# Optimization experiments

Hardware: AMD Instinct MI355X
Metric: run time of the kernel (lower is better)

## Reference

```python
import jax, jax.numpy as jnp
import numpy as np

S, B, D, H, K, M, MEM = 1024, 2, 1024, 16, 64, 4096, 1
T = (MEM + 1) * S  # key length = (mem_len+1)*seq_len


def setup_inputs() -> dict:
    key = jax.random.key(0)
    ks = jax.random.split(key, 16)

    def w(k, shape):  # N(0, 0.02) init as in the torch module
        return jax.random.normal(k, shape, dtype=jnp.float32) * 0.02

    x = jax.random.normal(ks[0], (S, B, D), dtype=jnp.float32)
    p = jax.random.normal(ks[1], (T, B, D), dtype=jnp.float32)
    memory = jax.random.normal(ks[2], (MEM * S, B, D), dtype=jnp.float32)
    u_bias = w(ks[3], (H, K))
    v_bias = w(ks[4], (H, K))
    # Transformer-XL causal mask: query s may attend to keys t <= mem_len*S + s
    t_idx = jnp.arange(T)[None, :]
    s_idx = jnp.arange(S)[:, None]
    mask = jnp.where(t_idx <= MEM * S + s_idx, 0.0, -1e9).astype(jnp.float32)[None]  # [1,S,T]
    return {
        "x": x, "p": p, "mask": mask, "memory": memory,
        "u_bias": u_bias, "v_bias": v_bias,
        "wq_w": w(ks[5], (H * K, D)), "wke_w": w(ks[6], (H * K, D)),
        "wkr_w": w(ks[7], (H * K, D)), "wv_w": w(ks[8], (H * K, D)),
        "wc_w": w(ks[9], (D, H * K)),
        "w1_w": w(ks[10], (M, D)), "w1_b": jnp.zeros((M,), jnp.float32),
        "w2_w": w(ks[11], (D, M)), "w2_b": jnp.zeros((D,), jnp.float32),
        "ln1_g": jnp.ones((D,), jnp.float32), "ln1_b": jnp.zeros((D,), jnp.float32),
        "ln2_g": jnp.ones((D,), jnp.float32), "ln2_b": jnp.zeros((D,), jnp.float32),
    }


def _layernorm(x, g, b, eps=1e-5):
    mu = jnp.mean(x, axis=-1, keepdims=True)
    var = jnp.mean(jnp.square(x - mu), axis=-1, keepdims=True)
    return (x - mu) / jnp.sqrt(var + eps) * g + b


def reference(x, p, mask, memory, u_bias, v_bias,
              wq_w, wke_w, wkr_w, wv_w, wc_w,
              w1_w, w1_b, w2_w, w2_b, ln1_g, ln1_b, ln2_g, ln2_b):
    s_len, b_sz, d = x.shape
    q = (x @ wq_w.T).reshape(s_len, b_sz, H, K)            # [S,B,H,K]
    x_mem = jnp.concatenate([memory, x], axis=0)           # [T,B,D]
    k_e = (x_mem @ wke_w.T).reshape(T, b_sz, H, K)         # content keys
    k_r = (p @ wkr_w.T).reshape(T, b_sz, H, K)             # relative-position keys
    v = (x_mem @ wv_w.T).reshape(T, b_sz, H, K)
    # AC: content score, BD: relative-position score (Transformer-XL)
    ac = jnp.einsum("sbhk,tbhk->bhst", q + u_bias, k_e)
    bd = jnp.einsum("sbhk,tbhk->bhst", q + v_bias, k_r)
    alpha = (ac + bd) / np.sqrt(K).astype(np.float32) + mask[:, None]  # [B,H,S,T]
    alpha = jax.nn.softmax(alpha, axis=-1)
    av = jnp.einsum("bhst,tbhk->sbhk", alpha, v).reshape(s_len, b_sz, H * K)
    u = av @ wc_w.T
    u = _layernorm(u + x, ln1_g, ln1_b)
    z = jax.nn.relu(u @ w1_w.T + w1_b) @ w2_w.T + w2_b
    z = _layernorm(z + u, ln2_g, ln2_b)
    return z
```

## Files before the change

kernel.cpp:

```cpp
#include <hip/hip_runtime.h>
#include <math.h>

#define S_LEN 1024
#define BATCH 2
#define DM 1024
#define NH 16
#define HD 64
#define FFN_DIM 4096
#define RQ 2048
#define RT 4096
#define T_LEN 2048
#define KROW 72
#define NPART 4
#define OPSTR 2097152L

typedef __attribute__((ext_vector_type(8))) short short8;
typedef __attribute__((ext_vector_type(4))) float f32x4;

__device__ __forceinline__ unsigned short f2bf(float f) {
    unsigned u = __builtin_bit_cast(unsigned, f);
    u += 0x7fffu + ((u >> 16) & 1u);
    return (unsigned short)(u >> 16);
}
__device__ __forceinline__ float bf2f(unsigned short s) { return __builtin_bit_cast(float, ((unsigned)s) << 16); }

#define GLD_LDS16(gptr, lptr)                                                                  \
    __builtin_amdgcn_global_load_lds((const __attribute__((address_space(1))) unsigned int*)(gptr), \
                                     (__attribute__((address_space(3))) unsigned int*)(lptr), 16, 0, 0)

__device__ __forceinline__ ushort4 cvt4(float4 v) {
    ushort4 o;
    o.x = f2bf(v.x); o.y = f2bf(v.y); o.z = f2bf(v.z); o.w = f2bf(v.w);
    return o;
}

__global__ void cast_all_kernel(const float* __restrict__ wq, const float* __restrict__ wke,
                                const float* __restrict__ wv, const float* __restrict__ wkr,
                                const float* __restrict__ wc, const float* __restrict__ w1,
                                const float* __restrict__ w2, const float* __restrict__ x,
                                const float* __restrict__ p, const float* __restrict__ mem,
                                unsigned short* __restrict__ wdst, unsigned short* __restrict__ xbf,
                                unsigned short* __restrict__ pbf, unsigned short* __restrict__ xm) {
    const long Q = 256 * 1024;
    const long W = 13 * Q;
    long i = (long)blockIdx.x * blockDim.x + threadIdx.x;
    if (i < W) {
        const float* src; long off;
        if      (i < 1 * Q) { src = wq;  off = 0; }
        else if (i < 2 * Q) { src = wke; off = 1 * Q; }
        else if (i < 3 * Q) { src = wv;  off = 2 * Q; }
        else if (i < 4 * Q) { src = wkr; off = 3 * Q; }
        else if (i < 5 * Q) { src = wc;  off = 4 * Q; }
        else if (i < 9 * Q) { src = w1;  off = 5 * Q; }
        else                { src = w2;  off = 9 * Q; }
        ((ushort4*)wdst)[i] = cvt4(((const float4*)src)[i - off]);
    } else if (i < W + 2 * Q) {
        long j = i - W;
        ((ushort4*)xbf)[j] = cvt4(((const float4*)x)[j]);
    } else if (i < W + 6 * Q) {
        long j = i - W - 2 * Q;
        ((ushort4*)pbf)[j] = cvt4(((const float4*)p)[j]);
    } else {
        long j = i - W - 6 * Q;
        float4 v = (j < 2 * Q) ? ((const float4*)mem)[j] : ((const float4*)x)[j - 2 * Q];
        ((ushort4*)xm)[j] = cvt4(v);
    }
}

#define BM 128
#define BN 128
#define GBK 64
#define PBK 32

__launch_bounds__(256)
__global__ void proj_fused(const unsigned short* __restrict__ xbf, const unsigned short* __restrict__ xmbf,
                           const unsigned short* __restrict__ pbf, const unsigned short* __restrict__ wqb,
                           const unsigned short* __restrict__ wkevb, const unsigned short* __restrict__ wkrb,
                           unsigned short* __restrict__ qo, unsigned short* __restrict__ keo,
                           unsigned short* __restrict__ vTo, unsigned short* __restrict__ kro) {
    __shared__ __align__(16) short As[BM * PBK];
    __shared__ __align__(16) short Bs[BN * PBK];
    const int id = blockIdx.x;
    const unsigned short *A, *B;
    unsigned short *Yb, *Yv = nullptr;
    int bx, by;
    if (id < 128)      { A = xbf;  B = wqb;   Yb = qo;  bx = id & 7;   by = id >> 3; }
    else if (id < 640) { int t = id - 128; A = xmbf; B = wkevb; Yb = keo; Yv = vTo;
                         bx = t & 15; by = t >> 4; }
    else               { int t = id - 640; A = pbf;  B = wkrb;  Yb = kro;
                         bx = t & 7;  by = t >> 3; }
    const int tid = threadIdx.x;
    const int w = tid >> 6, lane = tid & 63;
    const int row0 = by * BM, col0 = bx * BN;
    const int wr = (w >> 1) * 64, wcn = (w & 1) * 64;
    f32x4 acc[4][4] = {};
    const int lrow = lane & 15, quad = lane >> 4;
    for (int k0 = 0; k0 < DM; k0 += PBK) {
        __syncthreads();
#pragma unroll
        for (int i = 0; i < 2; ++i) {
            int c = w * 128 + i * 64 + lane;
            int row = c >> 2, kg = c & 3;
            int kl = (kg - (row >> 1)) & 3;
            GLD_LDS16(A + (long)(row0 + row) * DM + k0 + kl * 8, As + (w * 128 + i * 64) * 8);
            GLD_LDS16(B + (long)(col0 + row) * DM + k0 + kl * 8, Bs + (w * 128 + i * 64) * 8);
        }
        __syncthreads();
        short8 a[4], b[4];
#pragma unroll
        for (int mi = 0; mi < 4; ++mi) {
            int r = wr + mi * 16 + lrow;
            int ph = (quad + (r >> 1)) & 3;
            a[mi] = *(const short8*)&As[r * PBK + ph * 8];
        }
#pragma unroll
        for (int ni = 0; ni < 4; ++ni) {
            int r = wcn + ni * 16 + lrow;
            int ph = (quad + (r >> 1)) & 3;
            b[ni] = *(const short8*)&Bs[r * PBK + ph * 8];
        }
#pragma unroll
        for (int mi = 0; mi < 4; ++mi)
#pragma unroll
            for (int ni = 0; ni < 4; ++ni)
                acc[mi][ni] = __builtin_amdgcn_mfma_f32_16x16x32_bf16(a[mi], b[ni], acc[mi][ni], 0, 0, 0);
    }
    const int mb = row0 + wr + quad * 4;
    const int nb = col0 + wcn + lrow;
    const bool isv = (Yv != nullptr) && (col0 >= 1024);
#pragma unroll
    for (int mi = 0; mi < 4; ++mi)
#pragma unroll
        for (int ni = 0; ni < 4; ++ni) {
            const int r = mb + mi * 16, cc = nb + ni * 16;
#pragma unroll
            for (int reg = 0; reg < 4; ++reg) {
                float val = acc[mi][ni][reg];
                const int rf = r + reg;
                if (isv) {
                    int c2 = cc - 1024;
                    int t = rf >> 1, b2 = rf & 1;
                    int h2 = c2 >> 6, d2 = c2 & 63;
                    Yv[((long)(b2 * NH + h2) * HD + d2) * T_LEN + t] = f2bf(val);
                } else {
                    Yb[(long)rf * DM + cc] = f2bf(val);
                }
            }
        }
}

__launch_bounds__(256)
__global__ void gemm_mfma(const unsigned short* __restrict__ A, const unsigned short* __restrict__ B,
                          const float* __restrict__ bias,
                          float* __restrict__ of0, float* __restrict__ of1,
                          float* __restrict__ of2, float* __restrict__ of3,
                          unsigned short* __restrict__ Yb, int Kd, int N, int relu,
                          int klen) {
    __shared__ __align__(16) short As[BM * GBK];
    __shared__ __align__(16) short Bs[BN * GBK];
    const int nbx = N >> 7;
    const int cpx = gridDim.x >> 3;
    const int bid = ((blockIdx.x & 7) * cpx) + (blockIdx.x >> 3);
    const int per_z = nbx << 4;
    const int z = bid / per_z;
    const int r2 = bid - z * per_z;
    const int by = r2 / nbx, bx = r2 - by * nbx;
    const int tid = threadIdx.x;
    const int w = tid >> 6, lane = tid & 63;
    const int row0 = by * BM, col0 = bx * BN;
    const int kbeg = z * klen;
    const int wr = (w >> 1) * 64, wcn = (w & 1) * 64;
    f32x4 acc[4][4] = {};
    const int lrow = lane & 15, quad = lane >> 4;
    for (int k0 = kbeg; k0 < kbeg + klen; k0 += GBK) {
        __syncthreads();
#pragma unroll
        for (int i = 0; i < 4; ++i) {
            int c = i * 256 + tid;
            int row = c >> 3, ph = c & 7;
            int kl = (ph - row) & 7;
            GLD_LDS16(A + (long)(row0 + row) * Kd + k0 + kl * 8, As + (i * 256 + w * 64) * 8);
            GLD_LDS16(B + (long)(col0 + row) * Kd + k0 + kl * 8, Bs + (i * 256 + w * 64) * 8);
        }
        __syncthreads();
#pragma unroll
        for (int hh = 0; hh < 2; ++hh) {
            short8 a[4], b[4];
#pragma unroll
            for (int mi = 0; mi < 4; ++mi) {
                int r = wr + mi * 16 + lrow;
                int ph = (hh * 4 + quad + r) & 7;
                a[mi] = *(const short8*)&As[r * GBK + ph * 8];
            }
#pragma unroll
            for (int ni = 0; ni < 4; ++ni) {
                int r = wcn + ni * 16 + lrow;
                int ph = (hh * 4 + quad + r) & 7;
                b[ni] = *(const short8*)&Bs[r * GBK + ph * 8];
            }
#pragma unroll
            for (int mi = 0; mi < 4; ++mi)
#pragma unroll
                for (int ni = 0; ni < 4; ++ni)
                    acc[mi][ni] = __builtin_amdgcn_mfma_f32_16x16x32_bf16(a[mi], b[ni], acc[mi][ni], 0, 0, 0);
        }
    }
    const int mb = row0 + wr + quad * 4;
    const int nb = col0 + wcn + lrow;
    float* of = (z == 0) ? of0 : (z == 1) ? of1 : (z == 2) ? of2 : of3;
    float bb[4];
#pragma unroll
    for (int ni = 0; ni < 4; ++ni) bb[ni] = bias ? bias[nb + ni * 16] : 0.f;
#pragma unroll
    for (int mi = 0; mi < 4; ++mi)
#pragma unroll
        for (int ni = 0; ni < 4; ++ni) {
            const int r = mb + mi * 16, cc = nb + ni * 16;
#pragma unroll
            for (int reg = 0; reg < 4; ++reg) {
                float val = acc[mi][ni][reg] + bb[ni];
                if (relu) val = fmaxf(val, 0.f);
                if (Yb) Yb[(long)(r + reg) * N + cc] = f2bf(val);
                else    of[(long)(r + reg) * N + cc] = val;
            }
        }
}

__launch_bounds__(256)
__global__ void prep_kernel(const unsigned short* __restrict__ kr,
                            const float* __restrict__ ub, const float* __restrict__ vb,
                            unsigned short* __restrict__ ke_io, float* __restrict__ biasg) {
    const int r = blockIdx.x;
    const int tid = threadIdx.x;
    const int h = tid >> 4, seg = tid & 15;
    ushort4 keu = ((const ushort4*)(ke_io + (long)r * DM))[tid];
    ushort4 kru = ((const ushort4*)(kr + (long)r * DM))[tid];
    float ke0 = bf2f(keu.x), ke1 = bf2f(keu.y), ke2 = bf2f(keu.z), ke3 = bf2f(keu.w);
    float kr0 = bf2f(kru.x), kr1 = bf2f(kru.y), kr2 = bf2f(kru.z), kr3 = bf2f(kru.w);
    float4 u4 = ((const float4*)ub)[tid];
    float4 v4 = ((const float4*)vb)[tid];
    ushort4 s;
    s.x = f2bf((ke0 + kr0) * 0.125f); s.y = f2bf((ke1 + kr1) * 0.125f);
    s.z = f2bf((ke2 + kr2) * 0.125f); s.w = f2bf((ke3 + kr3) * 0.125f);
    ((ushort4*)(ke_io + (long)r * DM))[tid] = s;
    float part = u4.x * ke0 + u4.y * ke1 + u4.z * ke2 + u4.w * ke3
               + v4.x * kr0 + v4.y * kr1 + v4.z * kr2 + v4.w * kr3;
    part += __shfl_xor(part, 1);
    part += __shfl_xor(part, 2);
    part += __shfl_xor(part, 4);
    part += __shfl_xor(part, 8);
    if (seg == 0) {
        const int t = r >> 1, b = r & 1;
        biasg[(b * NH + h) * T_LEN + t] = part * 0.125f;
    }
}

__launch_bounds__(256)
__global__ void attn_mfma(const unsigned short* __restrict__ qg,
                          const unsigned short* __restrict__ ksum,
                          const unsigned short* __restrict__ vT,
                          const float* __restrict__ biasg,
                          float* __restrict__ Op01, float* __restrict__ Op2,
                          float* __restrict__ Op3, float2* __restrict__ mlout) {
    __shared__ __align__(16) unsigned short Ks[64 * KROW];
    __shared__ __align__(16) unsigned short Vs[64 * KROW];
    __shared__ __align__(16) unsigned short Ps[4][16 * KROW];
    const int bid0 = blockIdx.x;
    const int bid = (bid0 & 7) * 256 + (bid0 >> 3);
    const int part = bid >> 9, rid = bid & 511;
    const int stile = (rid & 15) ^ 15, h = (rid >> 4) & 15, b = rid >> 8;
    const int tid = threadIdx.x, w = tid >> 6, lane = tid & 63;
    const int L = lane & 15, quad = lane >> 4;
    const int qbase = stile * 64 + w * 16;
    short8 qf0, qf1;
    {
        const unsigned short* qp = qg + ((long)(qbase + L) * 2 + b) * DM + h * HD + quad * 8;
        qf0 = *(const short8*)(qp);
        qf1 = *(const short8*)(qp + 32);
    }
    f32x4 O[4] = {};
    float mrow[4] = {-1e30f, -1e30f, -1e30f, -1e30f};
    float lrow[4] = {0.f, 0.f, 0.f, 0.f};
    const int nch = 17 + stile;
    const float* bias_p = biasg + (long)(b * NH + h) * T_LEN;
    const unsigned short* ks_base = ksum + (long)b * DM + h * HD;
    const unsigned short* vt_base = vT + (long)(b * NH + h) * HD * T_LEN;
    const int c0 = tid, c1 = 256 + tid;
    const int row_a = c0 >> 3, seg_a = c0 & 7;
    const int row_b = c1 >> 3, seg_b = c1 & 7;
    uint4 pk0, pk1, pv0, pv1;
    float pb[4];
    {
        const int tf = part * 64;
        pk0 = *(const uint4*)(ks_base + (long)(tf + row_a) * 2 * DM + seg_a * 8);
        pk1 = *(const uint4*)(ks_base + (long)(tf + row_b) * 2 * DM + seg_b * 8);
        pv0 = *(const uint4*)(vt_base + (long)row_a * T_LEN + tf + seg_a * 8);
        pv1 = *(const uint4*)(vt_base + (long)row_b * T_LEN + tf + seg_b * 8);
#pragma unroll
        for (int kt = 0; kt < 4; ++kt) pb[kt] = bias_p[tf + kt * 16 + L];
    }
    for (int ch = part; ch < nch; ch += NPART) {
        const int t0 = ch * 64;
        __syncthreads();
        *(uint4*)&Ks[row_a * KROW + seg_a * 8] = pk0;
        *(uint4*)&Ks[row_b * KROW + seg_b * 8] = pk1;
        *(uint4*)&Vs[row_a * KROW + seg_a * 8] = pv0;
        *(uint4*)&Vs[row_b * KROW + seg_b * 8] = pv1;
        __syncthreads();
        const bool more = (ch + NPART < nch);
        float pbn[4];
        if (more) {
            const int t1 = t0 + NPART * 64;
            pk0 = *(const uint4*)(ks_base + (long)(t1 + row_a) * 2 * DM + seg_a * 8);
            pk1 = *(const uint4*)(ks_base + (long)(t1 + row_b) * 2 * DM + seg_b * 8);
            pv0 = *(const uint4*)(vt_base + (long)row_a * T_LEN + t1 + seg_a * 8);
            pv1 = *(const uint4*)(vt_base + (long)row_b * T_LEN + t1 + seg_b * 8);
#pragma unroll
            for (int kt = 0; kt < 4; ++kt) pbn[kt] = bias_p[t1 + kt * 16 + L];
        }
        f32x4 S[4] = {};
        __builtin_amdgcn_s_setprio(1);
#pragma unroll
        for (int kt = 0; kt < 4; ++kt) {
            short8 kb0 = *(const short8*)&Ks[(kt * 16 + L) * KROW + quad * 8];
            short8 kb1 = *(const short8*)&Ks[(kt * 16 + L) * KROW + 32 + quad * 8];
            S[kt] = __builtin_amdgcn_mfma_f32_16x16x32_bf16(qf0, kb0, S[kt], 0, 0, 0);
            S[kt] = __builtin_amdgcn_mfma_f32_16x16x32_bf16(qf1, kb1, S[kt], 0, 0, 0);
        }
        __builtin_amdgcn_s_setprio(0);
        float sc[4][4];
        float cm[4] = {-1e30f, -1e30f, -1e30f, -1e30f};
        if (ch != nch - 1) {
#pragma unroll
            for (int kt = 0; kt < 4; ++kt)
#pragma unroll
                for (int reg = 0; reg < 4; ++reg) {
                    float v = S[kt][reg] + pb[kt];
                    sc[kt][reg] = v;
                    cm[reg] = fmaxf(cm[reg], v);
                }
        } else {
#pragma unroll
            for (int kt = 0; kt < 4; ++kt)
#pragma unroll
                for (int reg = 0; reg < 4; ++reg) {
                    float v = S[kt][reg] + pb[kt];
                    if (t0 + kt * 16 + L > 1024 + qbase + quad * 4 + reg) v = -1e30f;
                    sc[kt][reg] = v;
                    cm[reg] = fmaxf(cm[reg], v);
                }
        }
#pragma unroll
        for (int off = 1; off < 16; off <<= 1)
#pragma unroll
            for (int reg = 0; reg < 4; ++reg) cm[reg] = fmaxf(cm[reg], __shfl_xor(cm[reg], off));
        float cf[4];
#pragma unroll
        for (int reg = 0; reg < 4; ++reg) {
            float mn = fmaxf(mrow[reg], cm[reg]);
            cf[reg] = __expf(mrow[reg] - mn);
            mrow[reg] = mn;
            lrow[reg] *= cf[reg];
        }
        float rs[4] = {0.f, 0.f, 0.f, 0.f};
#pragma unroll
        for (int kt = 0; kt < 4; ++kt)
#pragma unroll
            for (int reg = 0; reg < 4; ++reg) {
                float pv = __expf(sc[kt][reg] - mrow[reg]);
                rs[reg] += pv;
                Ps[w][(quad * 4 + reg) * KROW + kt * 16 + L] = f2bf(pv);
            }
#pragma unroll
        for (int off = 1; off < 16; off <<= 1)
#pragma unroll
            for (int reg = 0; reg < 4; ++reg) rs[reg] += __shfl_xor(rs[reg], off);
#pragma unroll
        for (int reg = 0; reg < 4; ++reg) lrow[reg] += rs[reg];
#pragma unroll
        for (int dt = 0; dt < 4; ++dt)
#pragma unroll
            for (int reg = 0; reg < 4; ++reg) O[dt][reg] *= cf[reg];
        short8 pa0 = *(const short8*)&Ps[w][L * KROW + quad * 8];
        short8 pa1 = *(const short8*)&Ps[w][L * KROW + 32 + quad * 8];
        __builtin_amdgcn_s_setprio(1);
#pragma unroll
        for (int dt = 0; dt < 4; ++dt) {
            short8 vb0 = *(const short8*)&Vs[(dt * 16 + L) * KROW + quad * 8];
            short8 vb1 = *(const short8*)&Vs[(dt * 16 + L) * KROW + 32 + quad * 8];
            O[dt] = __builtin_amdgcn_mfma_f32_16x16x32_bf16(pa0, vb0, O[dt], 0, 0, 0);
            O[dt] = __builtin_amdgcn_mfma_f32_16x16x32_bf16(pa1, vb1, O[dt], 0, 0, 0);
        }
        __builtin_amdgcn_s_setprio(0);
        if (more) {
#pragma unroll
            for (int kt = 0; kt < 4; ++kt) pb[kt] = pbn[kt];
        }
    }
    float* ob = (part == 0) ? Op01 : (part == 1) ? Op01 + OPSTR : (part == 2) ? Op2 : Op3;
    const long rbase = ((long)b * NH + h) * S_LEN;
#pragma unroll
    for (int reg = 0; reg < 4; ++reg) {
        const int s = qbase + quad * 4 + reg;
        float* op = ob + (rbase + s) * 64;
#pragma unroll
        for (int dt = 0; dt < 4; ++dt) op[dt * 16 + L] = O[dt][reg];
        if (L == 0) mlout[(long)part * 32768 + rbase + s] = make_float2(mrow[reg], lrow[reg]);
    }
}

__launch_bounds__(256)
__global__ void attn_combine(const float* __restrict__ Op01, const float* __restrict__ Op2,
                             const float* __restrict__ Op3, const float2* __restrict__ ml,
                             unsigned short* __restrict__ avout) {
    const int i = blockIdx.x * 256 + threadIdx.x;
    const int d4 = i & 15;
    const int row = i >> 4;
    const int s = row & 1023;
    const int bh = row >> 10;
    const int b = bh >> 4, h = bh & 15;
    float2 m0 = ml[row], m1 = ml[row + 32768], m2 = ml[row + 65536], m3 = ml[row + 98304];
    float m = fmaxf(fmaxf(m0.x, m1.x), fmaxf(m2.x, m3.x));
    float a0 = __expf(m0.x - m), a1 = __expf(m1.x - m);
    float a2 = __expf(m2.x - m), a3 = __expf(m3.x - m);
    float inv = 1.f / (a0 * m0.y + a1 * m1.y + a2 * m2.y + a3 * m3.y);
    a0 *= inv; a1 *= inv; a2 *= inv; a3 *= inv;
    float4 o0 = ((const float4*)Op01)[(long)row * 16 + d4];
    float4 o1 = ((const float4*)Op01)[((long)row + 32768) * 16 + d4];
    float4 o2 = ((const float4*)Op2)[(long)row * 16 + d4];
    float4 o3 = ((const float4*)Op3)[(long)row * 16 + d4];
    float4 o;
    o.x = a0 * o0.x + a1 * o1.x + a2 * o2.x + a3 * o3.x;
    o.y = a0 * o0.y + a1 * o1.y + a2 * o2.y + a3 * o3.y;
    o.z = a0 * o0.z + a1 * o1.z + a2 * o2.z + a3 * o3.z;
    o.w = a0 * o0.w + a1 * o1.w + a2 * o2.w + a3 * o3.w;
    *(ushort4*)(avout + ((long)s * 2 + b) * DM + h * HD + d4 * 4) = cvt4(o);
}

__launch_bounds__(256)
__global__ void ln_kernel(const float* __restrict__ a0, const float* __restrict__ a1,
                          const float* __restrict__ a2, const float* __restrict__ a3,
                          const float* __restrict__ cb, const float* __restrict__ r,
                          const float* __restrict__ g, const float* __restrict__ be,
                          float* __restrict__ out, unsigned short* __restrict__ outb) {
    const int row = blockIdx.x;
    const int tid = threadIdx.x;
    float4 xa = ((const float4*)(a0 + (long)row * DM))[tid];
    float4 x1 = ((const float4*)(a1 + (long)row * DM))[tid];
    float4 x2 = ((const float4*)(a2 + (long)row * DM))[tid];
    float4 x3 = ((const float4*)(a3 + (long)row * DM))[tid];
    xa.x += x1.x + x2.x + x3.x;
    xa.y += x1.y + x2.y + x3.y;
    xa.z += x1.z + x2.z + x3.z;
    xa.w += x1.w + x2.w + x3.w;
    if (cb) {
        float4 c4 = ((const float4*)cb)[tid];
        xa.x += c4.x; xa.y += c4.y; xa.z += c4.z; xa.w += c4.w;
    }
    float4 xr = ((const float4*)(r + (long)row * DM))[tid];
    float4 x = make_float4(xa.x + xr.x, xa.y + xr.y, xa.z + xr.z, xa.w + xr.w);
    float s1 = x.x + x.y + x.z + x.w;
    float s2 = x.x * x.x + x.y * x.y + x.z * x.z + x.w * x.w;
#pragma unroll
    for (int off = 32; off > 0; off >>= 1) {
        s1 += __shfl_down(s1, off);
        s2 += __shfl_down(s2, off);
    }
    __shared__ float w1s[4], w2s[4];
    const int wid = tid >> 6;
    if ((tid & 63) == 0) { w1s[wid] = s1; w2s[wid] = s2; }
    __syncthreads();
    float S1 = w1s[0] + w1s[1] + w1s[2] + w1s[3];
    float S2 = w2s[0] + w2s[1] + w2s[2] + w2s[3];
    float mu = S1 * (1.f / 1024.f);
    float var = S2 * (1.f / 1024.f) - mu * mu;
    float rstd = rsqrtf(var + 1e-5f);
    float4 gv = ((const float4*)g)[tid];
    float4 bv = ((const float4*)be)[tid];
    float4 o;
    o.x = (x.x - mu) * rstd * gv.x + bv.x;
    o.y = (x.y - mu) * rstd * gv.y + bv.y;
    o.z = (x.z - mu) * rstd * gv.z + bv.z;
    o.w = (x.w - mu) * rstd * gv.w + bv.w;
    ((float4*)(out + (long)row * DM))[tid] = o;
    if (outb) ((ushort4*)(outb + (long)row * DM))[tid] = cvt4(o);
}

extern "C" void kernel_launch(void* const* d_in, const int* in_sizes, int n_in,
                              void* d_out, int out_size, void* d_ws, size_t ws_size,
                              hipStream_t stream) {
    (void)in_sizes; (void)n_in; (void)out_size; (void)ws_size;
    const float* x    = (const float*)d_in[0];
    const float* p    = (const float*)d_in[1];
    const float* mem  = (const float*)d_in[3];
    const float* ub   = (const float*)d_in[4];
    const float* vb   = (const float*)d_in[5];
    const float* wq   = (const float*)d_in[6];
    const float* wke  = (const float*)d_in[7];
    const float* wkr  = (const float*)d_in[8];
    const float* wv   = (const float*)d_in[9];
    const float* wc   = (const float*)d_in[10];
    const float* w1   = (const float*)d_in[11];
    const float* w1b  = (const float*)d_in[12];
    const float* w2   = (const float*)d_in[13];
    const float* w2b  = (const float*)d_in[14];
    const float* ln1g = (const float*)d_in[15];
    const float* ln1b = (const float*)d_in[16];
    const float* ln2g = (const float*)d_in[17];
    const float* ln2b = (const float*)d_in[18];
    float* out = (float*)d_out;
    float* wsf = (float*)d_ws;
    unsigned short* ws16 = (unsigned short*)d_ws;

    const long HLF = 512 * 1024;
    const long M16 = 1024 * 1024;
    unsigned short* wq_bf   = ws16 + 0 * M16;
    unsigned short* wkev_bf = ws16 + 1 * M16;
    unsigned short* wkr_bf  = ws16 + 3 * M16;
    unsigned short* wc_bf   = ws16 + 4 * M16;
    unsigned short* w1_bf   = ws16 + 5 * M16;
    unsigned short* w2_bf   = ws16 + 9 * M16;
    unsigned short* x_bf   = (unsigned short*)(wsf + 13 * HLF);
    unsigned short* xm_bf  = (unsigned short*)(wsf + 15 * HLF);
    unsigned short* p_bf   = (unsigned short*)(wsf + 19 * HLF);
    unsigned short* q_bf   = (unsigned short*)(wsf + 23 * HLF);
    unsigned short* ke_bf  = (unsigned short*)(wsf + 25 * HLF);
    unsigned short* kr_bf  = (unsigned short*)(wsf + 29 * HLF);
    unsigned short* vT_bf  = (unsigned short*)(wsf + 33 * HLF);
    float* abias           = wsf + 37 * HLF;
    float2* mlpart         = (float2*)(wsf + 13 * HLF);
    float* Op01            = wsf + 15 * HLF;
    float* Op2             = wsf + 29 * HLF;
    float* Op3             = wsf + 0 * HLF;
    unsigned short* avb_bf = (unsigned short*)(wsf + 33 * HLF);
    float* t1p0            = wsf + 15 * HLF;
    float* t1p1            = wsf + 19 * HLF;
    float* t1p2            = wsf + 29 * HLF;
    float* t1p3            = wsf + 0 * HLF;
    float* u               = wsf + 25 * HLF;
    unsigned short* u_bf   = (unsigned short*)(wsf + 23 * HLF);
    unsigned short* z1_bf  = (unsigned short*)(wsf + 13 * HLF);
    float* t2p0            = wsf + 0 * HLF;
    float* t2p1            = wsf + 4 * HLF;
    float* t2p2            = wsf + 29 * HLF;
    float* t2p3            = wsf + 33 * HLF;

    cast_all_kernel<<<23552, 256, 0, stream>>>(wq, wke, wv, wkr, wc, w1, w2, x, p, mem,
                                               ws16, x_bf, p_bf, xm_bf);
    proj_fused<<<896, 256, 0, stream>>>(x_bf, xm_bf, p_bf, wq_bf, wkev_bf, wkr_bf,
                                        q_bf, ke_bf, vT_bf, kr_bf);
    prep_kernel<<<RT, 256, 0, stream>>>(kr_bf, ub, vb, ke_bf, abias);
    attn_mfma<<<512 * NPART, 256, 0, stream>>>(q_bf, ke_bf, vT_bf, abias, Op01, Op2, Op3, mlpart);
    attn_combine<<<2048, 256, 0, stream>>>(Op01, Op2, Op3, mlpart, avb_bf);
    gemm_mfma<<<512, 256, 0, stream>>>(avb_bf, wc_bf, nullptr, t1p0, t1p1, t1p2, t1p3,
                                       nullptr, DM, DM, 0, 256);
    ln_kernel<<<RQ, 256, 0, stream>>>(t1p0, t1p1, t1p2, t1p3, nullptr, x, ln1g, ln1b, u, u_bf);
    gemm_mfma<<<512, 256, 0, stream>>>(u_bf, w1_bf, w1b, nullptr, nullptr, nullptr, nullptr,
                                       z1_bf, DM, FFN_DIM, 1, DM);
    gemm_mfma<<<512, 256, 0, stream>>>(z1_bf, w2_bf, nullptr, t2p0, t2p1, t2p2, t2p3,
                                       nullptr, FFN_DIM, DM, 0, 1024);
    ln_kernel<<<RQ, 256, 0, stream>>>(t2p0, t2p1, t2p2, t2p3, w2b, u, ln2g, ln2b, out, nullptr);
}
```

Baseline: 372.1 us.

## Double-buffer LDS tiles in projection and generic GEMM kernels

Both MFMA GEMM kernels now keep two shared-memory tile buffers. The next K-slice is issued as async global-to-LDS loads into the other buffer before computing on the current one. This leaves one barrier per iteration instead of two and is meant to hide global load latency behind MFMA work. The generic GEMM's K-step drops from 64 to 32 so total LDS stays the same, which doubles its loop iterations and barrier count.

```diff
diff --git a/kernel.cpp b/kernel.cpp
--- a/kernel.cpp
+++ b/kernel.cpp
@@ -69,8 +69,7 @@
 
 #define BM 128
 #define BN 128
-#define GBK 64
-#define PBK 32
+#define BK 32
 
 __launch_bounds__(256)
 __global__ void proj_fused(const unsigned short* __restrict__ xbf, const unsigned short* __restrict__ xmbf,
@@ -78,8 +77,8 @@
                            const unsigned short* __restrict__ wkevb, const unsigned short* __restrict__ wkrb,
                            unsigned short* __restrict__ qo, unsigned short* __restrict__ keo,
                            unsigned short* __restrict__ vTo, unsigned short* __restrict__ kro) {
-    __shared__ __align__(16) short As[BM * PBK];
-    __shared__ __align__(16) short Bs[BN * PBK];
+    __shared__ __align__(16) short As[2][BM * BK];
+    __shared__ __align__(16) short Bs[2][BN * BK];
     const int id = blockIdx.x;
     const unsigned short *A, *B;
     unsigned short *Yb, *Yv = nullptr;
@@ -95,36 +94,42 @@
     const int wr = (w >> 1) * 64, wcn = (w & 1) * 64;
     f32x4 acc[4][4] = {};
     const int lrow = lane & 15, quad = lane >> 4;
-    for (int k0 = 0; k0 < DM; k0 += PBK) {
+    const int sc0 = w * 128 + lane, sc1 = w * 128 + 64 + lane;
+    const int srow0 = sc0 >> 2, skl0 = ((sc0 & 3) - (srow0 >> 1)) & 3;
+    const int srow1 = sc1 >> 2, skl1 = ((sc1 & 3) - (srow1 >> 1)) & 3;
+#define PSTAGE(bf, kk)                                                                       \
+    do {                                                                                     \
+        GLD_LDS16(A + (long)(row0 + srow0) * DM + (kk) + skl0 * 8, &As[bf][sc0 * 8]);        \
+        GLD_LDS16(B + (long)(col0 + srow0) * DM + (kk) + skl0 * 8, &Bs[bf][sc0 * 8]);        \
+        GLD_LDS16(A + (long)(row0 + srow1) * DM + (kk) + skl1 * 8, &As[bf][sc1 * 8]);        \
+        GLD_LDS16(B + (long)(col0 + srow1) * DM + (kk) + skl1 * 8, &Bs[bf][sc1 * 8]);        \
+    } while (0)
+    PSTAGE(0, 0);
+    int cur = 0;
+    for (int k0 = 0; k0 < DM; k0 += BK) {
         __syncthreads();
-#pragma unroll
-        for (int i = 0; i < 2; ++i) {
-            int c = w * 128 + i * 64 + lane;
-            int row = c >> 2, kg = c & 3;
-            int kl = (kg - (row >> 1)) & 3;
-            GLD_LDS16(A + (long)(row0 + row) * DM + k0 + kl * 8, As + (w * 128 + i * 64) * 8);
-            GLD_LDS16(B + (long)(col0 + row) * DM + k0 + kl * 8, Bs + (w * 128 + i * 64) * 8);
-        }
-        __syncthreads();
+        if (k0 + BK < DM) PSTAGE(cur ^ 1, k0 + BK);
         short8 a[4], b[4];
 #pragma unroll
         for (int mi = 0; mi < 4; ++mi) {
             int r = wr + mi * 16 + lrow;
             int ph = (quad + (r >> 1)) & 3;
-            a[mi] = *(const short8*)&As[r * PBK + ph * 8];
+            a[mi] = *(const short8*)&As[cur][r * BK + ph * 8];
         }
 #pragma unroll
         for (int ni = 0; ni < 4; ++ni) {
             int r = wcn + ni * 16 + lrow;
             int ph = (quad + (r >> 1)) & 3;
-            b[ni] = *(const short8*)&Bs[r * PBK + ph * 8];
+            b[ni] = *(const short8*)&Bs[cur][r * BK + ph * 8];
         }
 #pragma unroll
         for (int mi = 0; mi < 4; ++mi)
 #pragma unroll
             for (int ni = 0; ni < 4; ++ni)
                 acc[mi][ni] = __builtin_amdgcn_mfma_f32_16x16x32_bf16(a[mi], b[ni], acc[mi][ni], 0, 0, 0);
-    }
+        cur ^= 1;
+    }
+#undef PSTAGE
     const int mb = row0 + wr + quad * 4;
     const int nb = col0 + wcn + lrow;
     const bool isv = (Yv != nullptr) && (col0 >= 1024);
@@ -156,8 +161,8 @@
                           float* __restrict__ of2, float* __restrict__ of3,
                           unsigned short* __restrict__ Yb, int Kd, int N, int relu,
                           int klen) {
-    __shared__ __align__(16) short As[BM * GBK];
-    __shared__ __align__(16) short Bs[BN * GBK];
+    __shared__ __align__(16) short As[2][BM * BK];
+    __shared__ __align__(16) short Bs[2][BN * BK];
     const int nbx = N >> 7;
     const int cpx = gridDim.x >> 3;
     const int bid = ((blockIdx.x & 7) * cpx) + (blockIdx.x >> 3);
@@ -172,39 +177,42 @@
     const int wr = (w >> 1) * 64, wcn = (w & 1) * 64;
     f32x4 acc[4][4] = {};
     const int lrow = lane & 15, quad = lane >> 4;
-    for (int k0 = kbeg; k0 < kbeg + klen; k0 += GBK) {
+    const int sc0 = w * 128 + lane, sc1 = w * 128 + 64 + lane;
+    const int srow0 = sc0 >> 2, skl0 = ((sc0 & 3) - (srow0 >> 1)) & 3;
+    const int srow1 = sc1 >> 2, skl1 = ((sc1 & 3) - (srow1 >> 1)) & 3;
+#define GSTAGE(bf, kk)                                                                       \
+    do {                                                                                     \
+        GLD_LDS16(A + (long)(row0 + srow0) * Kd + (kk) + skl0 * 8, &As[bf][sc0 * 8]);        \
+        GLD_LDS16(B + (long)(col0 + srow0) * Kd + (kk) + skl0 * 8, &Bs[bf][sc0 * 8]);        \
+        GLD_LDS16(A + (long)(row0 + srow1) * Kd + (kk) + skl1 * 8, &As[bf][sc1 * 8]);        \
+        GLD_LDS16(B + (long)(col0 + srow1) * Kd + (kk) + skl1 * 8, &Bs[bf][sc1 * 8]);        \
+    } while (0)
+    GSTAGE(0, kbeg);
+    int cur = 0;
+    for (int k0 = kbeg; k0 < kbeg + klen; k0 += BK) {
         __syncthreads();
-#pragma unroll
-        for (int i = 0; i < 4; ++i) {
-            int c = i * 256 + tid;
-            int row = c >> 3, ph = c & 7;
-            int kl = (ph - row) & 7;
-            GLD_LDS16(A + (long)(row0 + row) * Kd + k0 + kl * 8, As + (i * 256 + w * 64) * 8);
-            GLD_LDS16(B + (long)(col0 + row) * Kd + k0 + kl * 8, Bs + (i * 256 + w * 64) * 8);
-        }
-        __syncthreads();
-#pragma unroll
-        for (int hh = 0; hh < 2; ++hh) {
-            short8 a[4], b[4];
-#pragma unroll
-            for (int mi = 0; mi < 4; ++mi) {
-                int r = wr + mi * 16 + lrow;
-                int ph = (hh * 4 + quad + r) & 7;
-                a[mi] = *(const short8*)&As[r * GBK + ph * 8];
-            }
-#pragma unroll
-            for (int ni = 0; ni < 4; ++ni) {
-                int r = wcn + ni * 16 + lrow;
-                int ph = (hh * 4 + quad + r) & 7;
-                b[ni] = *(const short8*)&Bs[r * GBK + ph * 8];
-            }
-#pragma unroll
-            for (int mi = 0; mi < 4; ++mi)
-#pragma unroll
-                for (int ni = 0; ni < 4; ++ni)
-                    acc[mi][ni] = __builtin_amdgcn_mfma_f32_16x16x32_bf16(a[mi], b[ni], acc[mi][ni], 0, 0, 0);
-        }
-    }
+        if (k0 + BK < kbeg + klen) GSTAGE(cur ^ 1, k0 + BK);
+        short8 a[4], b[4];
+#pragma unroll
+        for (int mi = 0; mi < 4; ++mi) {
+            int r = wr + mi * 16 + lrow;
+            int ph = (quad + (r >> 1)) & 3;
+            a[mi] = *(const short8*)&As[cur][r * BK + ph * 8];
+        }
+#pragma unroll
+        for (int ni = 0; ni < 4; ++ni) {
+            int r = wcn + ni * 16 + lrow;
+            int ph = (quad + (r >> 1)) & 3;
+            b[ni] = *(const short8*)&Bs[cur][r * BK + ph * 8];
+        }
+#pragma unroll
+        for (int mi = 0; mi < 4; ++mi)
+#pragma unroll
+            for (int ni = 0; ni < 4; ++ni)
+                acc[mi][ni] = __builtin_amdgcn_mfma_f32_16x16x32_bf16(a[mi], b[ni], acc[mi][ni], 0, 0, 0);
+        cur ^= 1;
+    }
+#undef GSTAGE
     const int mb = row0 + wr + quad * 4;
     const int nb = col0 + wcn + lrow;
     float* of = (z == 0) ? of0 : (z == 1) ? of1 : (z == 2) ? of2 : of3;
```

After: 381.9 us. 2.6% more time.

## Load K and V MFMA operands directly from global memory, dropping LDS staging

Applied to the files above, without the earlier changes.

The attention kernel no longer stages K and V tiles in shared memory with register prefetch and two barriers per chunk. Each wave now loads its MFMA B-operands for K and V straight from global memory, and V is loaded early so it overlaps the softmax. This removes the barriers and the LDS traffic. In exchange, every one of the four waves re-reads the same K/V tile from global memory or cache, and the software prefetch of the next chunk is gone, so load latency is more exposed.

```diff
diff --git a/kernel.cpp b/kernel.cpp
--- a/kernel.cpp
+++ b/kernel.cpp
@@ -262,8 +262,6 @@
                           const float* __restrict__ biasg,
                           float* __restrict__ Op01, float* __restrict__ Op2,
                           float* __restrict__ Op3, float2* __restrict__ mlout) {
-    __shared__ __align__(16) unsigned short Ks[64 * KROW];
-    __shared__ __align__(16) unsigned short Vs[64 * KROW];
     __shared__ __align__(16) unsigned short Ps[4][16 * KROW];
     const int bid0 = blockIdx.x;
     const int bid = (bid0 & 7) * 256 + (bid0 >> 3);
@@ -283,51 +281,31 @@
     float lrow[4] = {0.f, 0.f, 0.f, 0.f};
     const int nch = 17 + stile;
     const float* bias_p = biasg + (long)(b * NH + h) * T_LEN;
-    const unsigned short* ks_base = ksum + (long)b * DM + h * HD;
-    const unsigned short* vt_base = vT + (long)(b * NH + h) * HD * T_LEN;
-    const int c0 = tid, c1 = 256 + tid;
-    const int row_a = c0 >> 3, seg_a = c0 & 7;
-    const int row_b = c1 >> 3, seg_b = c1 & 7;
-    uint4 pk0, pk1, pv0, pv1;
-    float pb[4];
-    {
-        const int tf = part * 64;
-        pk0 = *(const uint4*)(ks_base + (long)(tf + row_a) * 2 * DM + seg_a * 8);
-        pk1 = *(const uint4*)(ks_base + (long)(tf + row_b) * 2 * DM + seg_b * 8);
-        pv0 = *(const uint4*)(vt_base + (long)row_a * T_LEN + tf + seg_a * 8);
-        pv1 = *(const uint4*)(vt_base + (long)row_b * T_LEN + tf + seg_b * 8);
-#pragma unroll
-        for (int kt = 0; kt < 4; ++kt) pb[kt] = bias_p[tf + kt * 16 + L];
-    }
+    const unsigned short* kL = ksum + (long)b * DM + h * HD + (long)L * 2 * DM + quad * 8;
+    const unsigned short* vL = vT + ((long)(b * NH + h) * HD + L) * T_LEN + quad * 8;
     for (int ch = part; ch < nch; ch += NPART) {
         const int t0 = ch * 64;
-        __syncthreads();
-        *(uint4*)&Ks[row_a * KROW + seg_a * 8] = pk0;
-        *(uint4*)&Ks[row_b * KROW + seg_b * 8] = pk1;
-        *(uint4*)&Vs[row_a * KROW + seg_a * 8] = pv0;
-        *(uint4*)&Vs[row_b * KROW + seg_b * 8] = pv1;
-        __syncthreads();
-        const bool more = (ch + NPART < nch);
-        float pbn[4];
-        if (more) {
-            const int t1 = t0 + NPART * 64;
-            pk0 = *(const uint4*)(ks_base + (long)(t1 + row_a) * 2 * DM + seg_a * 8);
-            pk1 = *(const uint4*)(ks_base + (long)(t1 + row_b) * 2 * DM + seg_b * 8);
-            pv0 = *(const uint4*)(vt_base + (long)row_a * T_LEN + t1 + seg_a * 8);
-            pv1 = *(const uint4*)(vt_base + (long)row_b * T_LEN + t1 + seg_b * 8);
-#pragma unroll
-            for (int kt = 0; kt < 4; ++kt) pbn[kt] = bias_p[t1 + kt * 16 + L];
-        }
         f32x4 S[4] = {};
+        float pb[4];
         __builtin_amdgcn_s_setprio(1);
 #pragma unroll
         for (int kt = 0; kt < 4; ++kt) {
-            short8 kb0 = *(const short8*)&Ks[(kt * 16 + L) * KROW + quad * 8];
-            short8 kb1 = *(const short8*)&Ks[(kt * 16 + L) * KROW + 32 + quad * 8];
+            const unsigned short* kp = kL + (long)(t0 + kt * 16) * 2 * DM;
+            short8 kb0 = *(const short8*)(kp);
+            short8 kb1 = *(const short8*)(kp + 32);
             S[kt] = __builtin_amdgcn_mfma_f32_16x16x32_bf16(qf0, kb0, S[kt], 0, 0, 0);
             S[kt] = __builtin_amdgcn_mfma_f32_16x16x32_bf16(qf1, kb1, S[kt], 0, 0, 0);
         }
         __builtin_amdgcn_s_setprio(0);
+        short8 vb0[4], vb1[4];
+#pragma unroll
+        for (int dt = 0; dt < 4; ++dt) {
+            const unsigned short* vp = vL + (long)dt * 16 * T_LEN + t0;
+            vb0[dt] = *(const short8*)(vp);
+            vb1[dt] = *(const short8*)(vp + 32);
+        }
+#pragma unroll
+        for (int kt = 0; kt < 4; ++kt) pb[kt] = bias_p[t0 + kt * 16 + L];
         float sc[4][4];
         float cm[4] = {-1e30f, -1e30f, -1e30f, -1e30f};
         if (ch != nch - 1) {
@@ -386,16 +364,10 @@
         __builtin_amdgcn_s_setprio(1);
 #pragma unroll
         for (int dt = 0; dt < 4; ++dt) {
-            short8 vb0 = *(const short8*)&Vs[(dt * 16 + L) * KROW + quad * 8];
-            short8 vb1 = *(const short8*)&Vs[(dt * 16 + L) * KROW + 32 + quad * 8];
-            O[dt] = __builtin_amdgcn_mfma_f32_16x16x32_bf16(pa0, vb0, O[dt], 0, 0, 0);
-            O[dt] = __builtin_amdgcn_mfma_f32_16x16x32_bf16(pa1, vb1, O[dt], 0, 0, 0);
+            O[dt] = __builtin_amdgcn_mfma_f32_16x16x32_bf16(pa0, vb0[dt], O[dt], 0, 0, 0);
+            O[dt] = __builtin_amdgcn_mfma_f32_16x16x32_bf16(pa1, vb1[dt], O[dt], 0, 0, 0);
         }
         __builtin_amdgcn_s_setprio(0);
-        if (more) {
-#pragma unroll
-            for (int kt = 0; kt < 4; ++kt) pb[kt] = pbn[kt];
-        }
     }
     float* ob = (part == 0) ? Op01 : (part == 1) ? Op01 + OPSTR : (part == 2) ? Op2 : Op3;
     const long rbase = ((long)b * NH + h) * S_LEN;
```

New measurement: 427.1 us. 14.8% more time.
